# Kernel tuning notes

Measured on AMD Instinct MI355X. Metric: run time of the kernel, lower is better.

The kernel has to match this reference:

```python
import jax, jax.numpy as jnp
import numpy as np

N = 16384
E = 524288
IN_DIM, H1, H2 = 256, 128, 64


def setup_inputs() -> dict:
    key = jax.random.key(0)
    ks = jax.random.split(key, 9)
    features = jax.random.normal(ks[0], (N, IN_DIM), dtype=jnp.float32)
    src = jax.random.randint(ks[1], (E,), 0, N, dtype=jnp.int32)
    dst = jax.random.randint(ks[2], (E,), 0, N, dtype=jnp.int32)
    s = 0.1
    W1 = jax.random.normal(ks[3], (IN_DIM, H1), dtype=jnp.float32) * s
    b1 = jnp.zeros((H1,), dtype=jnp.float32)
    W2 = jax.random.normal(ks[4], (H1, H1), dtype=jnp.float32) * s
    b2 = jnp.zeros((H1,), dtype=jnp.float32)
    W3 = jax.random.normal(ks[5], (H1, H2), dtype=jnp.float32) * s
    b3 = jnp.zeros((H2,), dtype=jnp.float32)
    return {"features": features, "src": src, "dst": dst,
            "W1": W1, "b1": b1, "W2": W2, "b2": b2, "W3": W3, "b3": b3}


def _degree_norms(src, dst):
    ones = jnp.ones(src.shape[0], dtype=jnp.float32)
    deg_out = jax.ops.segment_sum(ones, src, num_segments=N)
    deg_in = jax.ops.segment_sum(ones, dst, num_segments=N)
    # allow_zero_in_degree=True with norm='both': clamp degree to min 1
    norm_out = jax.lax.rsqrt(jnp.maximum(deg_out, 1.0))  # [N]
    norm_in = jax.lax.rsqrt(jnp.maximum(deg_in, 1.0))    # [N]
    return norm_out, norm_in


def _graph_conv(h, src, dst, norm_out, norm_in, W, b, relu):
    # DGL GraphConv, norm='both': D_in^{-1/2} A^T (D_out^{-1/2} h) W + b
    h = h * norm_out[:, None]
    msg = h[src]                                   # gather [E, d]
    agg = jax.ops.segment_sum(msg, dst, num_segments=N)  # scatter-add [N, d]
    out = agg * norm_in[:, None] @ W + b
    return jax.nn.relu(out) if relu else out


def reference(features, src, dst, W1, b1, W2, b2, W3, b3):
    norm_out, norm_in = _degree_norms(src, dst)
    h = _graph_conv(features, src, dst, norm_out, norm_in, W1, b1, True)
    h = _graph_conv(h, src, dst, norm_out, norm_in, W2, b2, True)
    z = _graph_conv(h, src, dst, norm_out, norm_in, W3, b3, False)  # [N, H2]
    adj_rec = jax.nn.sigmoid(z @ z.T)  # [N, N]
    return adj_rec, z
```

## Files before the change

kernel.cpp:

```cpp
#include <hip/hip_runtime.h>
#include <hip/hip_bf16.h>

#define NN 16384
#define EE 524288

constexpr int D0 = 256, D1 = 128, D2 = 64;

typedef __attribute__((ext_vector_type(8))) short short8;
typedef __attribute__((ext_vector_type(4))) float f32x4;


__global__ __launch_bounds__(256) void count_deg_kernel(
    const int* __restrict__ src, const int* __restrict__ dst,
    int* __restrict__ deg_out, int* __restrict__ deg_in) {
  int e = blockIdx.x * 256 + threadIdx.x;
  if (e < EE) {
    atomicAdd(&deg_out[src[e]], 1);
    atomicAdd(&deg_in[dst[e]], 1);
  }
}

__global__ __launch_bounds__(256) void norm_kernel(
    const int* __restrict__ deg_out, const int* __restrict__ deg_in,
    float* __restrict__ norm_out, float* __restrict__ norm_in) {
  int i = blockIdx.x * 256 + threadIdx.x;
  if (i < NN) {
    norm_out[i] = rsqrtf(fmaxf((float)deg_out[i], 1.0f));
    norm_in[i]  = rsqrtf(fmaxf((float)deg_in[i], 1.0f));
  }
}

__global__ __launch_bounds__(256) void prefix_kernel(
    const int* __restrict__ deg_in, int* __restrict__ row_ptr,
    int* __restrict__ cursor) {
  __shared__ int part[256];
  int t = threadIdx.x;
  int base = t * 64;
  int s = 0;
  for (int j = 0; j < 64; ++j) s += deg_in[base + j];
  part[t] = s;
  __syncthreads();
  for (int off = 1; off < 256; off <<= 1) {
    int add = (t >= off) ? part[t - off] : 0;
    __syncthreads();
    part[t] += add;
    __syncthreads();
  }
  int run = (t == 0) ? 0 : part[t - 1];
  for (int j = 0; j < 64; ++j) {
    row_ptr[base + j] = run;
    cursor[base + j] = run;
    run += deg_in[base + j];
  }
  if (t == 255) row_ptr[NN] = run;
}

__global__ __launch_bounds__(256) void fill_csr_kernel(
    const int* __restrict__ src, const int* __restrict__ dst,
    int* __restrict__ cursor, int* __restrict__ csr_src) {
  int e = blockIdx.x * 256 + threadIdx.x;
  if (e < EE) {
    int pos = atomicAdd(&cursor[dst[e]], 1);
    csr_src[pos] = src[e];
  }
}


template<int DIN, int DOUT>
__global__ __launch_bounds__(256) void gemm_kernel(
    const float* __restrict__ h, const float* __restrict__ W,
    const float* __restrict__ norm_out, float* __restrict__ t) {
  constexpr int W4 = DOUT / 4;
  constexpr int RG = 256 / W4;
  constexpr int RPT = 32 / RG;
  __shared__ float A[32][DIN];
  int tid = threadIdx.x;
  int r0 = blockIdx.x * 32;
  constexpr int NF4 = 32 * DIN / 4;
  for (int q = tid; q < NF4; q += 256) {
    int r = q / (DIN / 4);
    int c = q % (DIN / 4);
    float4 x = *(const float4*)&h[(size_t)(r0 + r) * DIN + c * 4];
    float no = norm_out[r0 + r];
    x.x *= no; x.y *= no; x.z *= no; x.w *= no;
    *(float4*)&A[r][c * 4] = x;
  }
  __syncthreads();
  int c4 = tid % W4;
  int rg = tid / W4;
  float4 acc[RPT];
#pragma unroll
  for (int j = 0; j < RPT; ++j) acc[j] = make_float4(0.f, 0.f, 0.f, 0.f);
  const float* Wp = W + c4 * 4;
#pragma unroll 2
  for (int k = 0; k < DIN; ++k) {
    float4 w = *(const float4*)&Wp[(size_t)k * DOUT];
#pragma unroll
    for (int j = 0; j < RPT; ++j) {
      float a = A[rg + j * RG][k];
      acc[j].x += a * w.x; acc[j].y += a * w.y;
      acc[j].z += a * w.z; acc[j].w += a * w.w;
    }
  }
#pragma unroll
  for (int j = 0; j < RPT; ++j)
    *(float4*)&t[(size_t)(r0 + rg + j * RG) * DOUT + c4 * 4] = acc[j];
}


template<int DOUT, bool RELU, bool WRITE_BF16>
__global__ __launch_bounds__(256) void gather_kernel(
    const float* __restrict__ t, const float* __restrict__ bias,
    const float* __restrict__ norm_in, const int* __restrict__ row_ptr,
    const int* __restrict__ csr, float* __restrict__ out,
    ushort* __restrict__ zb) {
  constexpr int W4 = DOUT / 4;
  constexpr int S = 256 / W4;
  __shared__ float4 red[256];
  int tid = threadIdx.x;
  int c4 = tid % W4, slot = tid / W4;
  int v = blockIdx.x;
  int k0 = row_ptr[v], k1 = row_ptr[v + 1];
  float4 acc = make_float4(0.f, 0.f, 0.f, 0.f);
  for (int k = k0 + slot; k < k1; k += S) {
    int s = csr[k];
    float4 m = *(const float4*)&t[(size_t)s * DOUT + c4 * 4];
    acc.x += m.x; acc.y += m.y; acc.z += m.z; acc.w += m.w;
  }
  red[tid] = acc;
  __syncthreads();
  if (tid < W4) {
    float4 a = red[tid];
#pragma unroll
    for (int s = 1; s < S; ++s) {
      float4 b = red[s * W4 + tid];
      a.x += b.x; a.y += b.y; a.z += b.z; a.w += b.w;
    }
    float ni = norm_in[v];
    float4 b4 = *(const float4*)&bias[tid * 4];
    a.x = a.x * ni + b4.x; a.y = a.y * ni + b4.y;
    a.z = a.z * ni + b4.z; a.w = a.w * ni + b4.w;
    if (RELU) {
      a.x = fmaxf(a.x, 0.f); a.y = fmaxf(a.y, 0.f);
      a.z = fmaxf(a.z, 0.f); a.w = fmaxf(a.w, 0.f);
    }
    *(float4*)&out[(size_t)v * DOUT + tid * 4] = a;
    if (WRITE_BF16) {
      float vals[4] = {a.x, a.y, a.z, a.w};
#pragma unroll
      for (int i = 0; i < 4; ++i) {
        __hip_bfloat16 hb = __float2bfloat16(vals[i]);
        zb[(size_t)v * DOUT + tid * 4 + i] = *reinterpret_cast<ushort*>(&hb);
      }
    }
  }
}


__global__ __launch_bounds__(256) void adj_mfma_kernel(
    const ushort* __restrict__ zb, float* __restrict__ C) {
  __shared__ ushort ZR[128 * 64];
  __shared__ ushort ZC[128 * 64];
  int t = threadIdx.x;
  int bx = blockIdx.x & 127, by = blockIdx.x >> 7;
  int row0 = by * 128, col0 = bx * 128;
  {
    int r = t >> 1;
    int ub = (t & 1) * 4;
    const float4* zr = (const float4*)(zb + (size_t)(row0 + r) * 64);
    const float4* zc = (const float4*)(zb + (size_t)(col0 + r) * 64);
    float4* LR = (float4*)ZR;
    float4* LC = (float4*)ZC;
#pragma unroll
    for (int u = 0; u < 4; ++u) {
      int sw = (ub + u) ^ (r & 7);
      LR[r * 8 + sw] = zr[ub + u];
      LC[r * 8 + sw] = zc[ub + u];
    }
  }
  __syncthreads();
  int l = t & 63, w = t >> 6;
  int wy = w >> 1, wx = w & 1;
  int lr = l & 15, lg = l >> 4;
  f32x4 acc[4][4];
#pragma unroll
  for (int i = 0; i < 4; ++i)
#pragma unroll
    for (int j = 0; j < 4; ++j) acc[i][j] = (f32x4){0.f, 0.f, 0.f, 0.f};

#pragma unroll
  for (int ks = 0; ks < 2; ++ks) {
    short8 af[4], bf_[4];
    int u = ks * 4 + lg;
#pragma unroll
    for (int i = 0; i < 4; ++i) {
      int ar = wy * 64 + i * 16 + lr;
      af[i] = *(const short8*)&ZR[ar * 64 + ((u ^ (ar & 7)) << 3)];
      int ac = wx * 64 + i * 16 + lr;
      bf_[i] = *(const short8*)&ZC[ac * 64 + ((u ^ (ac & 7)) << 3)];
    }
#pragma unroll
    for (int i = 0; i < 4; ++i)
#pragma unroll
      for (int j = 0; j < 4; ++j)
        acc[i][j] = __builtin_amdgcn_mfma_f32_16x16x32_bf16(
            af[i], bf_[j], acc[i][j], 0, 0, 0);
  }

#pragma unroll
  for (int i = 0; i < 4; ++i) {
#pragma unroll
    for (int q = 0; q < 4; ++q) {
      int row = row0 + wy * 64 + i * 16 + lg * 4 + q;
#pragma unroll
      for (int j = 0; j < 4; ++j) {
        int col = col0 + wx * 64 + j * 16 + lr;
        float x = acc[i][j][q];
        C[(size_t)row * NN + col] = 1.0f / (1.0f + __expf(-x));
      }
    }
  }
}


extern "C" void kernel_launch(void* const* d_in, const int* in_sizes, int n_in,
                              void* d_out, int out_size, void* d_ws, size_t ws_size,
                              hipStream_t stream) {
  const float* features = (const float*)d_in[0];
  const int* src = (const int*)d_in[1];
  const int* dst = (const int*)d_in[2];
  const float* W1 = (const float*)d_in[3];
  const float* b1 = (const float*)d_in[4];
  const float* W2 = (const float*)d_in[5];
  const float* b2 = (const float*)d_in[6];
  const float* W3 = (const float*)d_in[7];
  const float* b3 = (const float*)d_in[8];

  float* outp = (float*)d_out;
  float* adj = outp;
  float* z = outp + (size_t)NN * NN;

  float* tA = adj;
  float* tB = adj + (size_t)NN * 128;
  float* tC = adj + (size_t)2 * NN * 128;

  float* wsf = (float*)d_ws;
  float* norm_out = wsf;
  float* norm_in = wsf + NN;
  int* deg_out = (int*)(wsf + 2 * NN);
  int* deg_in = deg_out + NN;
  int* row_ptr = deg_in + NN;
  int* cursor = row_ptr + NN + 256;
  int* csr_src = cursor + NN;
  ushort* zb = (ushort*)(csr_src + EE);

  hipMemsetAsync(deg_out, 0, 2 * NN * sizeof(int), stream);
  count_deg_kernel<<<EE / 256, 256, 0, stream>>>(src, dst, deg_out, deg_in);
  norm_kernel<<<NN / 256, 256, 0, stream>>>(deg_out, deg_in, norm_out, norm_in);
  prefix_kernel<<<1, 256, 0, stream>>>(deg_in, row_ptr, cursor);
  fill_csr_kernel<<<EE / 256, 256, 0, stream>>>(src, dst, cursor, csr_src);

  gemm_kernel<D0, D1><<<NN / 32, 256, 0, stream>>>(features, W1, norm_out, tA);
  gather_kernel<D1, true, false><<<NN, 256, 0, stream>>>(
      tA, b1, norm_in, row_ptr, csr_src, tB, nullptr);
  gemm_kernel<D1, D1><<<NN / 32, 256, 0, stream>>>(tB, W2, norm_out, tC);
  gather_kernel<D1, true, false><<<NN, 256, 0, stream>>>(
      tC, b2, norm_in, row_ptr, csr_src, tA, nullptr);
  gemm_kernel<D1, D2><<<NN / 32, 256, 0, stream>>>(tA, W3, norm_out, tB);
  gather_kernel<D2, false, true><<<NN, 256, 0, stream>>>(
      tB, b3, norm_in, row_ptr, csr_src, z, zb);

  adj_mfma_kernel<<<(NN / 128) * (NN / 128), 256, 0, stream>>>(zb, adj);
}
```

Measured before the change: 483.0 us.

## Store layer 1-2 transformed features in bf16 and vectorize adjacency sigmoid stores

The first two GEMMs now write their transformed features as bf16, and new gather kernels read 8 bf16 values per thread, which halves the bytes moved by the random-access neighbor gathers. The adjacency MFMA swaps its operand order so each lane holds four consecutive columns. This lets the sigmoid output be written as float4 stores, and it uses a hardware reciprocal instead of a divide. Storing intermediates in bf16 adds rounding error to the hidden layers, and the z output may drift from the fp32 reference.

```diff
diff --git a/kernel.cpp b/kernel.cpp
--- a/kernel.cpp
+++ b/kernel.cpp
@@ -8,6 +8,12 @@
 
 typedef __attribute__((ext_vector_type(8))) short short8;
 typedef __attribute__((ext_vector_type(4))) float f32x4;
+
+__device__ __forceinline__ float b2f(ushort u) {
+  union { unsigned int i; float f; } x;
+  x.i = ((unsigned int)u) << 16;
+  return x.f;
+}
 
 
 __global__ __launch_bounds__(256) void count_deg_kernel(
@@ -66,10 +72,11 @@
 }
 
 
-template<int DIN, int DOUT>
+template<int DIN, int DOUT, bool OBF16>
 __global__ __launch_bounds__(256) void gemm_kernel(
     const float* __restrict__ h, const float* __restrict__ W,
-    const float* __restrict__ norm_out, float* __restrict__ t) {
+    const float* __restrict__ norm_out, float* __restrict__ tf,
+    ushort* __restrict__ tb) {
   constexpr int W4 = DOUT / 4;
   constexpr int RG = 256 / W4;
   constexpr int RPT = 32 / RG;
@@ -103,13 +110,74 @@
     }
   }
 #pragma unroll
-  for (int j = 0; j < RPT; ++j)
-    *(float4*)&t[(size_t)(r0 + rg + j * RG) * DOUT + c4 * 4] = acc[j];
-}
-
-
-template<int DOUT, bool RELU, bool WRITE_BF16>
-__global__ __launch_bounds__(256) void gather_kernel(
+  for (int j = 0; j < RPT; ++j) {
+    size_t row = (size_t)(r0 + rg + j * RG);
+    if (OBF16) {
+      ushort4 o;
+      __hip_bfloat16 h0 = __float2bfloat16(acc[j].x);
+      __hip_bfloat16 h1 = __float2bfloat16(acc[j].y);
+      __hip_bfloat16 h2 = __float2bfloat16(acc[j].z);
+      __hip_bfloat16 h3 = __float2bfloat16(acc[j].w);
+      o.x = *reinterpret_cast<ushort*>(&h0);
+      o.y = *reinterpret_cast<ushort*>(&h1);
+      o.z = *reinterpret_cast<ushort*>(&h2);
+      o.w = *reinterpret_cast<ushort*>(&h3);
+      *(ushort4*)&tb[row * DOUT + c4 * 4] = o;
+    } else {
+      *(float4*)&tf[row * DOUT + c4 * 4] = acc[j];
+    }
+  }
+}
+
+
+template<int DOUT, bool RELU>
+__global__ __launch_bounds__(256) void gather_bf16_kernel(
+    const ushort* __restrict__ t, const float* __restrict__ bias,
+    const float* __restrict__ norm_in, const int* __restrict__ row_ptr,
+    const int* __restrict__ csr, float* __restrict__ out) {
+  constexpr int G8 = DOUT / 8;
+  constexpr int S = 256 / G8;
+  __shared__ float red[S][G8][8];
+  int tid = threadIdx.x;
+  int c8 = tid % G8, slot = tid / G8;
+  int v = blockIdx.x;
+  int k0 = row_ptr[v], k1 = row_ptr[v + 1];
+  float a[8];
+#pragma unroll
+  for (int i = 0; i < 8; ++i) a[i] = 0.f;
+  for (int k = k0 + slot; k < k1; k += S) {
+    int s = csr[k];
+    short8 m = *(const short8*)&t[(size_t)s * DOUT + c8 * 8];
+#pragma unroll
+    for (int i = 0; i < 8; ++i) a[i] += b2f((ushort)m[i]);
+  }
+#pragma unroll
+  for (int i = 0; i < 8; ++i) red[slot][c8][i] = a[i];
+  __syncthreads();
+#pragma unroll
+  for (int s = S / 2; s >= 1; s >>= 1) {
+    if (slot < s) {
+#pragma unroll
+      for (int i = 0; i < 8; ++i) red[slot][c8][i] += red[slot + s][c8][i];
+    }
+    __syncthreads();
+  }
+  if (tid < G8) {
+    float ni = norm_in[v];
+    float o[8];
+#pragma unroll
+    for (int i = 0; i < 8; ++i) {
+      o[i] = red[0][tid][i] * ni + bias[tid * 8 + i];
+      if (RELU) o[i] = fmaxf(o[i], 0.f);
+    }
+    *(float4*)&out[(size_t)v * DOUT + tid * 8] = make_float4(o[0], o[1], o[2], o[3]);
+    *(float4*)&out[(size_t)v * DOUT + tid * 8 + 4] = make_float4(o[4], o[5], o[6], o[7]);
+  }
+}
+
+
+template<int DOUT, bool RELU>
+__global__ __launch_bounds__(256) void gather_f32_kernel(
     const float* __restrict__ t, const float* __restrict__ bias,
     const float* __restrict__ norm_in, const int* __restrict__ row_ptr,
     const int* __restrict__ csr, float* __restrict__ out,
@@ -145,14 +213,17 @@
       a.z = fmaxf(a.z, 0.f); a.w = fmaxf(a.w, 0.f);
     }
     *(float4*)&out[(size_t)v * DOUT + tid * 4] = a;
-    if (WRITE_BF16) {
-      float vals[4] = {a.x, a.y, a.z, a.w};
-#pragma unroll
-      for (int i = 0; i < 4; ++i) {
-        __hip_bfloat16 hb = __float2bfloat16(vals[i]);
-        zb[(size_t)v * DOUT + tid * 4 + i] = *reinterpret_cast<ushort*>(&hb);
-      }
-    }
+    float vals[4] = {a.x, a.y, a.z, a.w};
+    ushort4 ob;
+    __hip_bfloat16 h0 = __float2bfloat16(vals[0]);
+    __hip_bfloat16 h1 = __float2bfloat16(vals[1]);
+    __hip_bfloat16 h2 = __float2bfloat16(vals[2]);
+    __hip_bfloat16 h3 = __float2bfloat16(vals[3]);
+    ob.x = *reinterpret_cast<ushort*>(&h0);
+    ob.y = *reinterpret_cast<ushort*>(&h1);
+    ob.z = *reinterpret_cast<ushort*>(&h2);
+    ob.w = *reinterpret_cast<ushort*>(&h3);
+    *(ushort4*)&zb[(size_t)v * DOUT + tid * 4] = ob;
   }
 }
 
@@ -204,20 +275,22 @@
 #pragma unroll
       for (int j = 0; j < 4; ++j)
         acc[i][j] = __builtin_amdgcn_mfma_f32_16x16x32_bf16(
-            af[i], bf_[j], acc[i][j], 0, 0, 0);
+            bf_[j], af[i], acc[i][j], 0, 0, 0);
   }
 
 #pragma unroll
   for (int i = 0; i < 4; ++i) {
-#pragma unroll
-    for (int q = 0; q < 4; ++q) {
-      int row = row0 + wy * 64 + i * 16 + lg * 4 + q;
-#pragma unroll
-      for (int j = 0; j < 4; ++j) {
-        int col = col0 + wx * 64 + j * 16 + lr;
-        float x = acc[i][j][q];
-        C[(size_t)row * NN + col] = 1.0f / (1.0f + __expf(-x));
-      }
+    int crow = row0 + wy * 64 + i * 16 + lr;
+    float* Crow = C + (size_t)crow * NN;
+#pragma unroll
+    for (int j = 0; j < 4; ++j) {
+      int ccol = col0 + wx * 64 + j * 16 + lg * 4;
+      float4 o;
+      o.x = __builtin_amdgcn_rcpf(1.0f + __expf(-acc[i][j][0]));
+      o.y = __builtin_amdgcn_rcpf(1.0f + __expf(-acc[i][j][1]));
+      o.z = __builtin_amdgcn_rcpf(1.0f + __expf(-acc[i][j][2]));
+      o.w = __builtin_amdgcn_rcpf(1.0f + __expf(-acc[i][j][3]));
+      *(float4*)&Crow[ccol] = o;
     }
   }
 }
@@ -240,9 +313,9 @@
   float* adj = outp;
   float* z = outp + (size_t)NN * NN;
 
-  float* tA = adj;
-  float* tB = adj + (size_t)NN * 128;
-  float* tC = adj + (size_t)2 * NN * 128;
+  ushort* tb = (ushort*)adj;
+  float* hbuf = adj + (size_t)NN * 64;
+  float* t3 = adj + (size_t)NN * 192;
 
   float* wsf = (float*)d_ws;
   float* norm_out = wsf;
@@ -260,15 +333,18 @@
   prefix_kernel<<<1, 256, 0, stream>>>(deg_in, row_ptr, cursor);
   fill_csr_kernel<<<EE / 256, 256, 0, stream>>>(src, dst, cursor, csr_src);
 
-  gemm_kernel<D0, D1><<<NN / 32, 256, 0, stream>>>(features, W1, norm_out, tA);
-  gather_kernel<D1, true, false><<<NN, 256, 0, stream>>>(
-      tA, b1, norm_in, row_ptr, csr_src, tB, nullptr);
-  gemm_kernel<D1, D1><<<NN / 32, 256, 0, stream>>>(tB, W2, norm_out, tC);
-  gather_kernel<D1, true, false><<<NN, 256, 0, stream>>>(
-      tC, b2, norm_in, row_ptr, csr_src, tA, nullptr);
-  gemm_kernel<D1, D2><<<NN / 32, 256, 0, stream>>>(tA, W3, norm_out, tB);
-  gather_kernel<D2, false, true><<<NN, 256, 0, stream>>>(
-      tB, b3, norm_in, row_ptr, csr_src, z, zb);
+  gemm_kernel<D0, D1, true><<<NN / 32, 256, 0, stream>>>(
+      features, W1, norm_out, nullptr, tb);
+  gather_bf16_kernel<D1, true><<<NN, 256, 0, stream>>>(
+      tb, b1, norm_in, row_ptr, csr_src, hbuf);
+  gemm_kernel<D1, D1, true><<<NN / 32, 256, 0, stream>>>(
+      hbuf, W2, norm_out, nullptr, tb);
+  gather_bf16_kernel<D1, true><<<NN, 256, 0, stream>>>(
+      tb, b2, norm_in, row_ptr, csr_src, hbuf);
+  gemm_kernel<D1, D2, false><<<NN / 32, 256, 0, stream>>>(
+      hbuf, W3, norm_out, t3, nullptr);
+  gather_f32_kernel<D2, false><<<NN, 256, 0, stream>>>(
+      t3, b3, norm_in, row_ptr, csr_src, z, zb);
 
   adj_mfma_kernel<<<(NN / 128) * (NN / 128), 256, 0, stream>>>(zb, adj);
 }
```

New measurement: 478.1 us. About the same (-1.0%).
